# Kernel optimization log

Measured on AMD Instinct MI355X. Metric: run time of the kernel, lower is better.

The kernel has to match this reference:

```python
import jax, jax.numpy as jnp
import numpy as np

N_NODES = 100_000
N_EDGES = 1_600_000
N_FEAT = 128
N_HID = 64
N_CLASS = 10
N_LAYERS = 3
N_GRAPHS = 1000


def _linear_init(key, fan_in, fan_out):
    kw, kb = jax.random.split(key)
    s = 1.0 / np.sqrt(fan_in)
    w = jax.random.uniform(kw, (fan_in, fan_out), minval=-s, maxval=s, dtype=jnp.float32)
    b = jax.random.uniform(kb, (fan_out,), minval=-s, maxval=s, dtype=jnp.float32)
    return w, b


def setup_inputs() -> dict:
    key = jax.random.key(0)
    ks = jax.random.split(key, 16)
    x = jax.random.normal(ks[0], (N_NODES, N_FEAT), dtype=jnp.float32)
    edge_index = jax.random.randint(ks[1], (2, N_EDGES), 0, N_NODES, dtype=jnp.int64)
    batch = jnp.sort(jax.random.randint(ks[2], (N_NODES,), 0, N_GRAPHS, dtype=jnp.int64))

    pre_w, pre_b = _linear_init(ks[3], N_FEAT, N_HID)
    w1s, b1s, w2s, b2s = [], [], [], []
    for l in range(N_LAYERS):
        w1, b1 = _linear_init(jax.random.fold_in(ks[4], 2 * l), N_HID, N_HID)
        w2, b2 = _linear_init(jax.random.fold_in(ks[4], 2 * l + 1), N_HID, N_HID)
        w1s.append(w1); b1s.append(b1); w2s.append(w2); b2s.append(b2)
    post_w, post_b = _linear_init(ks[5], N_HID, N_HID)
    ro_w, ro_b = _linear_init(ks[6], N_HID, N_CLASS)

    return {
        "x": x, "edge_index": edge_index, "batch": batch,
        "pre_w": pre_w, "pre_b": pre_b,
        "conv_w1": jnp.stack(w1s), "conv_b1": jnp.stack(b1s),
        "conv_w2": jnp.stack(w2s), "conv_b2": jnp.stack(b2s),
        "post_w": post_w, "post_b": post_b,
        "ro_w": ro_w, "ro_b": ro_b,
    }


def reference(x, edge_index, batch, pre_w, pre_b, conv_w1, conv_b1, conv_w2, conv_b2, post_w, post_b, ro_w, ro_b):
    src = edge_index[0]  # message source (x_j)
    dst = edge_index[1]  # message target

    h = x @ pre_w + pre_b  # [N, H]
    for l in range(N_LAYERS):
        # GINConv, eps=0: MLP((1+eps)*h_i + sum_{j in N(i)} h_j)
        agg = jax.ops.segment_sum(h[src], dst, num_segments=N_NODES)
        z = h + agg
        z = jax.nn.relu(z @ conv_w1[l] + conv_b1[l]) @ conv_w2[l] + conv_b2[l]
        h = jax.nn.relu(z)  # dropout is identity in eval mode

    g = jax.ops.segment_sum(h, batch, num_segments=N_GRAPHS)  # global_add_pool [G, H]
    g = jax.nn.relu(g @ post_w + post_b)
    logits = g @ ro_w + ro_b
    return jax.nn.log_softmax(logits, axis=1)
```

## Files before the change

### kernel.cpp

```cpp
#include <hip/hip_runtime.h>
#include <math.h>

#define N_NODES  100000
#define N_FEAT   128
#define N_HID    64
#define N_CLASS  10
#define N_GRAPHS 1000
#define N_EDGES  1600000
#define NTILES   1563
#define BLK_N    128
#define NT2      782
#define HF_GROUPS 8
#define HF_RANGE 12500
#define HF_BLOCKS 2048
#define CSR_STRIDE 64
#define EMAX_LDS 32
#define APITCH 72

typedef int iv4 __attribute__((ext_vector_type(4)));
typedef __attribute__((ext_vector_type(8))) __bf16 bf16x8;
typedef __attribute__((ext_vector_type(4))) float f32x4;

__device__ __forceinline__ float bflo(unsigned u) { return __uint_as_float(u << 16); }
__device__ __forceinline__ float bfhi(unsigned u) { return __uint_as_float(u & 0xffff0000u); }
__device__ __forceinline__ unsigned bf_rne(float f) {
    unsigned u = __float_as_uint(f);
    return (u + 0x7fffu + ((u >> 16) & 1u)) >> 16;
}
__device__ __forceinline__ unsigned pack2(float a, float b) {
    return bf_rne(a) | (bf_rne(b) << 16);
}

__global__ __launch_bounds__(256, 4) void pre_kernel(
    const float* __restrict__ x, const float* __restrict__ W,
    const float* __restrict__ b, uint2* __restrict__ h)
{
    __shared__ float xs[64][68];
    __shared__ float ws[64][68];
    const int tid = threadIdx.x;
    const int tx = tid & 15, ty = tid >> 4;
    const int n0 = blockIdx.x * 64;

    float acc[4][4];
#pragma unroll
    for (int i = 0; i < 4; ++i)
#pragma unroll
        for (int j = 0; j < 4; ++j) acc[i][j] = 0.f;

    for (int p = 0; p < 2; ++p) {
        __syncthreads();
#pragma unroll
        for (int t = 0; t < 4; ++t) {
            const int idx = t * 256 + tid;
            const int m = idx >> 4, kv = idx & 15;
            float4 v = make_float4(0.f, 0.f, 0.f, 0.f);
            if (n0 + m < N_NODES)
                v = *(const float4*)(x + (size_t)(n0 + m) * N_FEAT + p * 64 + kv * 4);
            *(float4*)&xs[m][kv * 4] = v;
            *(float4*)&ws[m][kv * 4] =
                *(const float4*)(W + (size_t)(p * 64 + m) * N_HID + kv * 4);
        }
        __syncthreads();
#pragma unroll 2
        for (int k4 = 0; k4 < 16; ++k4) {
            float4 a[4], bb[4];
#pragma unroll
            for (int i = 0; i < 4; ++i)
                a[i] = *(const float4*)&xs[ty + 16 * i][k4 * 4];
#pragma unroll
            for (int j = 0; j < 4; ++j)
                bb[j] = *(const float4*)&ws[k4 * 4 + j][tx * 4];
#pragma unroll
            for (int i = 0; i < 4; ++i) {
                const float* ap = (const float*)&a[i];
#pragma unroll
                for (int j = 0; j < 4; ++j) {
                    const float* bp = (const float*)&bb[j];
#pragma unroll
                    for (int c = 0; c < 4; ++c)
                        acc[i][c] = fmaf(ap[j], bp[c], acc[i][c]);
                }
            }
        }
    }

    const float4 bias = *(const float4*)(b + tx * 4);
#pragma unroll
    for (int i = 0; i < 4; ++i) {
        const int node = n0 + ty + 16 * i;
        if (node < N_NODES) {
            h[(size_t)node * 16 + tx] = make_uint2(
                pack2(acc[i][0] + bias.x, acc[i][1] + bias.y),
                pack2(acc[i][2] + bias.z, acc[i][3] + bias.w));
        }
    }
}

__global__ __launch_bounds__(256) void hist_fill_kernel(
    const int* __restrict__ ei, int* __restrict__ deg, int* __restrict__ csr)
{
    const int r   = blockIdx.x & (HF_GROUPS - 1);
    const int g   = blockIdx.x >> 3;
    const int lo  = r * HF_RANGE;
    const int hi  = lo + HF_RANGE;
    const int gsz = (gridDim.x >> 3) * blockDim.x;
    const int t0  = g * blockDim.x + threadIdx.x;
    const iv4* dst4 = (const iv4*)(ei + N_EDGES);
    for (int q = t0; q < N_EDGES / 4; q += gsz) {
        const iv4 d = __builtin_nontemporal_load(dst4 + q);
        const int e0 = q * 4;
        if (d.x >= lo && d.x < hi) {
            int p = atomicAdd(&deg[d.x], 1);
            if (p < CSR_STRIDE)
                csr[d.x * CSR_STRIDE + p] = __builtin_nontemporal_load(ei + e0);
        }
        if (d.y >= lo && d.y < hi) {
            int p = atomicAdd(&deg[d.y], 1);
            if (p < CSR_STRIDE)
                csr[d.y * CSR_STRIDE + p] = __builtin_nontemporal_load(ei + e0 + 1);
        }
        if (d.z >= lo && d.z < hi) {
            int p = atomicAdd(&deg[d.z], 1);
            if (p < CSR_STRIDE)
                csr[d.z * CSR_STRIDE + p] = __builtin_nontemporal_load(ei + e0 + 2);
        }
        if (d.w >= lo && d.w < hi) {
            int p = atomicAdd(&deg[d.w], 1);
            if (p < CSR_STRIDE)
                csr[d.w * CSR_STRIDE + p] = __builtin_nontemporal_load(ei + e0 + 3);
        }
    }
}

__global__ __launch_bounds__(512, 6) void gather_mlp_kernel(
    const uint2* __restrict__ hin, uint2* __restrict__ hout,
    const int* __restrict__ csr, const int* __restrict__ deg,
    const float* __restrict__ W1, const float* __restrict__ b1,
    const float* __restrict__ W2, const float* __restrict__ b2)
{
    __shared__ unsigned short asb[BLK_N][APITCH];
    __shared__ unsigned short wsb[N_HID][APITCH];
    __shared__ int sdeg[BLK_N];
    const int tid = threadIdx.x;
    const int tx = tid & 15, ty = tid >> 4;
    const int sub = tx;
    const int n0 = blockIdx.x * BLK_N;

#pragma unroll
    for (int t = 0; t < 8; ++t) {
        const int idx = t * 512 + tid;
        wsb[idx & 63][idx >> 6] = (unsigned short)bf_rne(W1[idx]);
    }
    if (tid < BLK_N) {
        const int node = n0 + tid;
        sdeg[tid] = (node < N_NODES) ? deg[node] : 0;
    }
#pragma unroll
    for (int t = 0; t < 2; ++t) {
        const int idx = t * 512 + tid;
        const int r = idx >> 3, s4 = idx & 7;
        const int node = n0 + r;
        int4 v = make_int4(0, 0, 0, 0);
        if (node < N_NODES)
            v = *(const int4*)(csr + (size_t)node * CSR_STRIDE + s4 * 4);
        *(int4*)((char*)&asb[r][0] + s4 * 16) = v;
    }
    __syncthreads();

    for (int pp = 0; pp < 2; ++pp) {
        const int rA = ty + 64 * pp;
        const int rB = rA + 32;
        const int nodeA = n0 + rA;
        const int nodeB = n0 + rB;
        float aAx = 0.f, aAy = 0.f, aAz = 0.f, aAw = 0.f;
        float bAx = 0.f, bAy = 0.f, bAz = 0.f, bAw = 0.f;
        float aBx = 0.f, aBy = 0.f, aBz = 0.f, aBw = 0.f;
        float bBx = 0.f, bBy = 0.f, bBz = 0.f, bBw = 0.f;
        int nA = 0, nB = 0;
        if (nodeA < N_NODES) {
            nA = sdeg[rA]; nA = nA > CSR_STRIDE ? CSR_STRIDE : nA;
            const uint2 s = hin[(size_t)nodeA * 16 + sub];
            aAx = bflo(s.x); aAy = bfhi(s.x); aAz = bflo(s.y); aAw = bfhi(s.y);
        }
        if (nodeB < N_NODES) {
            nB = sdeg[rB]; nB = nB > CSR_STRIDE ? CSR_STRIDE : nB;
            const uint2 s = hin[(size_t)nodeB * 16 + sub];
            aBx = bflo(s.x); aBy = bfhi(s.x); aBz = bflo(s.y); aBw = bfhi(s.y);
        }
        const int nnA = nA > EMAX_LDS ? EMAX_LDS : nA;
        const int nnB = nB > EMAX_LDS ? EMAX_LDS : nB;
        const int* epA = (const int*)&asb[rA][0];
        const int* epB = (const int*)&asb[rB][0];
        const int mx = nnA > nnB ? nnA : nnB;
        for (int eb = 0; eb < mx; eb += 8) {
            uint2 rvA[8], rvB[8];
            const bool doA = eb < nnA;
            const bool doB = eb < nnB;
            if (doA) {
#pragma unroll
                for (int u = 0; u < 8; ++u) {
                    const int idx = eb + u;
                    const int cl = idx < nnA ? idx : nnA - 1;
                    rvA[u] = hin[(size_t)epA[cl] * 16 + sub];
                }
            }
            if (doB) {
#pragma unroll
                for (int u = 0; u < 8; ++u) {
                    const int idx = eb + u;
                    const int cl = idx < nnB ? idx : nnB - 1;
                    rvB[u] = hin[(size_t)epB[cl] * 16 + sub];
                }
            }
            if (doA) {
#pragma unroll
                for (int u = 0; u < 8; u += 2) {
                    if (eb + u < nnA) {
                        aAx += bflo(rvA[u].x); aAy += bfhi(rvA[u].x);
                        aAz += bflo(rvA[u].y); aAw += bfhi(rvA[u].y);
                    }
                    if (eb + u + 1 < nnA) {
                        bAx += bflo(rvA[u + 1].x); bAy += bfhi(rvA[u + 1].x);
                        bAz += bflo(rvA[u + 1].y); bAw += bfhi(rvA[u + 1].y);
                    }
                }
            }
            if (doB) {
#pragma unroll
                for (int u = 0; u < 8; u += 2) {
                    if (eb + u < nnB) {
                        aBx += bflo(rvB[u].x); aBy += bfhi(rvB[u].x);
                        aBz += bflo(rvB[u].y); aBw += bfhi(rvB[u].y);
                    }
                    if (eb + u + 1 < nnB) {
                        bBx += bflo(rvB[u + 1].x); bBy += bfhi(rvB[u + 1].x);
                        bBz += bflo(rvB[u + 1].y); bBw += bfhi(rvB[u + 1].y);
                    }
                }
            }
        }
        for (int t = EMAX_LDS; t < nA; ++t) {
            const int s0 = csr[(size_t)nodeA * CSR_STRIDE + t];
            const uint2 a = hin[(size_t)s0 * 16 + sub];
            aAx += bflo(a.x); aAy += bfhi(a.x);
            aAz += bflo(a.y); aAw += bfhi(a.y);
        }
        for (int t = EMAX_LDS; t < nB; ++t) {
            const int s0 = csr[(size_t)nodeB * CSR_STRIDE + t];
            const uint2 a = hin[(size_t)s0 * 16 + sub];
            aBx += bflo(a.x); aBy += bfhi(a.x);
            aBz += bflo(a.y); aBw += bfhi(a.y);
        }
        *(uint2*)((char*)&asb[rA][0] + sub * 8) = make_uint2(
            pack2(aAx + bAx, aAy + bAy), pack2(aAz + bAz, aAw + bAw));
        *(uint2*)((char*)&asb[rB][0] + sub * 8) = make_uint2(
            pack2(aBx + bBx, aBy + bBy), pack2(aBz + bBz, aBw + bBw));
    }
    __syncthreads();

    const int wave = tid >> 6;
    const int lane = tid & 63;
    const int lr = lane & 15;
    const int lg = lane >> 4;
    const f32x4 vzero = {0.f, 0.f, 0.f, 0.f};

    f32x4 acc[4] = {vzero, vzero, vzero, vzero};
    {
        const char* ar = (const char*)&asb[wave * 16 + lr][0] + lg * 16;
        const bf16x8 a0 = *(const bf16x8*)ar;
        const bf16x8 a1 = *(const bf16x8*)(ar + 64);
#pragma unroll
        for (int cb = 0; cb < 4; ++cb) {
            const char* br = (const char*)&wsb[cb * 16 + lr][0] + lg * 16;
            const bf16x8 w0 = *(const bf16x8*)br;
            const bf16x8 w1 = *(const bf16x8*)(br + 64);
            acc[cb] = __builtin_amdgcn_mfma_f32_16x16x32_bf16(a0, w0, acc[cb], 0, 0, 0);
            acc[cb] = __builtin_amdgcn_mfma_f32_16x16x32_bf16(a1, w1, acc[cb], 0, 0, 0);
        }
    }
#pragma unroll
    for (int cb = 0; cb < 4; ++cb) {
        const float bias = b1[cb * 16 + lr];
#pragma unroll
        for (int rg = 0; rg < 4; ++rg) {
            const float v = fmaxf(acc[cb][rg] + bias, 0.f);
            asb[wave * 16 + lg * 4 + rg][cb * 16 + lr] = (unsigned short)bf_rne(v);
        }
    }
    __syncthreads();
#pragma unroll
    for (int t = 0; t < 8; ++t) {
        const int idx = t * 512 + tid;
        wsb[idx & 63][idx >> 6] = (unsigned short)bf_rne(W2[idx]);
    }
    __syncthreads();

#pragma unroll
    for (int cb = 0; cb < 4; ++cb) acc[cb] = vzero;
    {
        const char* ar = (const char*)&asb[wave * 16 + lr][0] + lg * 16;
        const bf16x8 a0 = *(const bf16x8*)ar;
        const bf16x8 a1 = *(const bf16x8*)(ar + 64);
#pragma unroll
        for (int cb = 0; cb < 4; ++cb) {
            const char* br = (const char*)&wsb[cb * 16 + lr][0] + lg * 16;
            const bf16x8 w0 = *(const bf16x8*)br;
            const bf16x8 w1 = *(const bf16x8*)(br + 64);
            acc[cb] = __builtin_amdgcn_mfma_f32_16x16x32_bf16(a0, w0, acc[cb], 0, 0, 0);
            acc[cb] = __builtin_amdgcn_mfma_f32_16x16x32_bf16(a1, w1, acc[cb], 0, 0, 0);
        }
    }
#pragma unroll
    for (int cb = 0; cb < 4; ++cb) {
        const float bias = b2[cb * 16 + lr];
#pragma unroll
        for (int rg = 0; rg < 4; ++rg) {
            const float v = fmaxf(acc[cb][rg] + bias, 0.f);
            asb[wave * 16 + lg * 4 + rg][cb * 16 + lr] = (unsigned short)bf_rne(v);
        }
    }
    __syncthreads();

#pragma unroll
    for (int t = 0; t < 4; ++t) {
        const int idx = t * 512 + tid;
        const int m = idx >> 4, kv = idx & 15;
        if (n0 + m < N_NODES)
            hout[(size_t)(n0 + m) * 16 + kv] =
                *(const uint2*)((const char*)&asb[m][0] + kv * 8);
    }
}

__global__ __launch_bounds__(256) void pool_head_kernel(
    const unsigned short* __restrict__ h, const int* __restrict__ batch,
    const float* __restrict__ Wp, const float* __restrict__ bp,
    const float* __restrict__ Wr, const float* __restrict__ br,
    float* __restrict__ out)
{
    const int graph = blockIdx.x;
    int l = 0, r = N_NODES;
    while (l < r) { int m = (l + r) >> 1; if (batch[m] < graph) l = m + 1; else r = m; }
    const int lo = l;
    r = N_NODES;
    while (l < r) { int m = (l + r) >> 1; if (batch[m] < graph + 1) l = m + 1; else r = m; }
    const int hi = l;

    const int lane = threadIdx.x & 63;
    const int wave = threadIdx.x >> 6;
    float acc = 0.0f;
    for (int i = lo + wave; i < hi; i += 4)
        acc += __uint_as_float(((unsigned)h[(size_t)i * N_HID + lane]) << 16);
    __shared__ float sacc[4][N_HID];
    sacc[wave][lane] = acc;
    __syncthreads();
    if (wave != 0) return;

    const float gv = sacc[0][lane] + sacc[1][lane] + sacc[2][lane] + sacc[3][lane];
    float acc2 = bp[lane];
#pragma unroll
    for (int k = 0; k < N_HID; ++k) {
        const float gk = __int_as_float(
            __builtin_amdgcn_readlane(__float_as_int(gv), k));
        acc2 = fmaf(gk, Wp[k * N_HID + lane], acc2);
    }
    const float y = fmaxf(acc2, 0.f);

    float logit = (lane < N_CLASS) ? br[lane] : 0.f;
#pragma unroll
    for (int k = 0; k < N_HID; ++k) {
        const float yk = __int_as_float(
            __builtin_amdgcn_readlane(__float_as_int(y), k));
        if (lane < N_CLASS)
            logit = fmaf(yk, Wr[k * N_CLASS + lane], logit);
    }

    __shared__ float slog[N_CLASS];
    if (lane < N_CLASS) slog[lane] = logit;
    if (lane < N_CLASS) {
        float m = -INFINITY;
#pragma unroll
        for (int c = 0; c < N_CLASS; ++c) m = fmaxf(m, slog[c]);
        float sum = 0.0f;
#pragma unroll
        for (int c = 0; c < N_CLASS; ++c) sum += expf(slog[c] - m);
        out[(size_t)graph * N_CLASS + lane] = logit - m - logf(sum);
    }
}

extern "C" void kernel_launch(void* const* d_in, const int* in_sizes, int n_in,
                              void* d_out, int out_size, void* d_ws, size_t ws_size,
                              hipStream_t stream)
{
    const float* x       = (const float*)d_in[0];
    const int*   ei      = (const int*)d_in[1];
    const int*   batch   = (const int*)d_in[2];
    const float* pre_w   = (const float*)d_in[3];
    const float* pre_b   = (const float*)d_in[4];
    const float* conv_w1 = (const float*)d_in[5];
    const float* conv_b1 = (const float*)d_in[6];
    const float* conv_w2 = (const float*)d_in[7];
    const float* conv_b2 = (const float*)d_in[8];
    const float* post_w  = (const float*)d_in[9];
    const float* post_b  = (const float*)d_in[10];
    const float* ro_w    = (const float*)d_in[11];
    const float* ro_b    = (const float*)d_in[12];
    float* out = (float*)d_out;

    uint2* h0   = (uint2*)d_ws;
    uint2* h1   = h0 + (size_t)N_NODES * 16;
    int*   deg  = (int*)(h1 + (size_t)N_NODES * 16);
    int*   csr  = deg + N_NODES;

    (void)hipMemsetAsync(deg, 0, N_NODES * sizeof(int), stream);

    pre_kernel<<<NTILES, 256, 0, stream>>>(x, pre_w, pre_b, h0);
    hist_fill_kernel<<<HF_BLOCKS, 256, 0, stream>>>(ei, deg, csr);

    gather_mlp_kernel<<<NT2, 512, 0, stream>>>(
        h0, h1, csr, deg,
        conv_w1, conv_b1, conv_w2, conv_b2);
    gather_mlp_kernel<<<NT2, 512, 0, stream>>>(
        h1, h0, csr, deg,
        conv_w1 + N_HID * N_HID, conv_b1 + N_HID,
        conv_w2 + N_HID * N_HID, conv_b2 + N_HID);
    gather_mlp_kernel<<<NT2, 512, 0, stream>>>(
        h0, h1, csr, deg,
        conv_w1 + 2 * N_HID * N_HID, conv_b1 + 2 * N_HID,
        conv_w2 + 2 * N_HID * N_HID, conv_b2 + 2 * N_HID);

    pool_head_kernel<<<N_GRAPHS, 256, 0, stream>>>(
        (const unsigned short*)h1, batch, post_w, post_b, ro_w, ro_b, out);
}
```

Measured before the change: 379.1 us.

## Fuse pre-linear and CSR histogram fill into one interleaved kernel

Merges the pre-projection GEMM and the edge histogram/CSR fill into a single launch, interleaving the two block types so the compute-bound projection and the atomic-heavy CSR build share the GPU at the same time. The pre-projection is rewritten so each wavefront holds 16 node rows in registers and broadcasts x values with readlane, with no LDS tiling. This drops a launch and its tail, and lets the two independent phases overlap. The cost is higher register pressure and a less efficient per-wave FMA scheme: there are 16 readlanes per k, and W is reloaded from global memory per k.

```diff
diff --git a/kernel.cpp b/kernel.cpp
--- a/kernel.cpp
+++ b/kernel.cpp
@@ -13,6 +13,8 @@
 #define HF_GROUPS 8
 #define HF_RANGE 12500
 #define HF_BLOCKS 2048
+#define HF_GSZ   65536
+#define FUSED_BLOCKS (2*NTILES + (HF_BLOCKS - NTILES))
 #define CSR_STRIDE 64
 #define EMAX_LDS 32
 #define APITCH 72
@@ -31,103 +33,84 @@
     return bf_rne(a) | (bf_rne(b) << 16);
 }
 
-__global__ __launch_bounds__(256, 4) void pre_kernel(
+__global__ __launch_bounds__(256, 6) void pre_hist_kernel(
     const float* __restrict__ x, const float* __restrict__ W,
-    const float* __restrict__ b, uint2* __restrict__ h)
-{
-    __shared__ float xs[64][68];
-    __shared__ float ws[64][68];
-    const int tid = threadIdx.x;
-    const int tx = tid & 15, ty = tid >> 4;
-    const int n0 = blockIdx.x * 64;
-
-    float acc[4][4];
-#pragma unroll
-    for (int i = 0; i < 4; ++i)
-#pragma unroll
-        for (int j = 0; j < 4; ++j) acc[i][j] = 0.f;
-
-    for (int p = 0; p < 2; ++p) {
-        __syncthreads();
-#pragma unroll
-        for (int t = 0; t < 4; ++t) {
-            const int idx = t * 256 + tid;
-            const int m = idx >> 4, kv = idx & 15;
-            float4 v = make_float4(0.f, 0.f, 0.f, 0.f);
-            if (n0 + m < N_NODES)
-                v = *(const float4*)(x + (size_t)(n0 + m) * N_FEAT + p * 64 + kv * 4);
-            *(float4*)&xs[m][kv * 4] = v;
-            *(float4*)&ws[m][kv * 4] =
-                *(const float4*)(W + (size_t)(p * 64 + m) * N_HID + kv * 4);
-        }
-        __syncthreads();
-#pragma unroll 2
-        for (int k4 = 0; k4 < 16; ++k4) {
-            float4 a[4], bb[4];
-#pragma unroll
-            for (int i = 0; i < 4; ++i)
-                a[i] = *(const float4*)&xs[ty + 16 * i][k4 * 4];
-#pragma unroll
-            for (int j = 0; j < 4; ++j)
-                bb[j] = *(const float4*)&ws[k4 * 4 + j][tx * 4];
-#pragma unroll
-            for (int i = 0; i < 4; ++i) {
-                const float* ap = (const float*)&a[i];
-#pragma unroll
-                for (int j = 0; j < 4; ++j) {
-                    const float* bp = (const float*)&bb[j];
-#pragma unroll
-                    for (int c = 0; c < 4; ++c)
-                        acc[i][c] = fmaf(ap[j], bp[c], acc[i][c]);
-                }
-            }
-        }
-    }
-
-    const float4 bias = *(const float4*)(b + tx * 4);
-#pragma unroll
-    for (int i = 0; i < 4; ++i) {
-        const int node = n0 + ty + 16 * i;
-        if (node < N_NODES) {
-            h[(size_t)node * 16 + tx] = make_uint2(
-                pack2(acc[i][0] + bias.x, acc[i][1] + bias.y),
-                pack2(acc[i][2] + bias.z, acc[i][3] + bias.w));
-        }
-    }
-}
-
-__global__ __launch_bounds__(256) void hist_fill_kernel(
+    const float* __restrict__ b, unsigned short* __restrict__ h16,
     const int* __restrict__ ei, int* __restrict__ deg, int* __restrict__ csr)
 {
-    const int r   = blockIdx.x & (HF_GROUPS - 1);
-    const int g   = blockIdx.x >> 3;
-    const int lo  = r * HF_RANGE;
-    const int hi  = lo + HF_RANGE;
-    const int gsz = (gridDim.x >> 3) * blockDim.x;
-    const int t0  = g * blockDim.x + threadIdx.x;
-    const iv4* dst4 = (const iv4*)(ei + N_EDGES);
-    for (int q = t0; q < N_EDGES / 4; q += gsz) {
-        const iv4 d = __builtin_nontemporal_load(dst4 + q);
-        const int e0 = q * 4;
-        if (d.x >= lo && d.x < hi) {
-            int p = atomicAdd(&deg[d.x], 1);
-            if (p < CSR_STRIDE)
-                csr[d.x * CSR_STRIDE + p] = __builtin_nontemporal_load(ei + e0);
-        }
-        if (d.y >= lo && d.y < hi) {
-            int p = atomicAdd(&deg[d.y], 1);
-            if (p < CSR_STRIDE)
-                csr[d.y * CSR_STRIDE + p] = __builtin_nontemporal_load(ei + e0 + 1);
-        }
-        if (d.z >= lo && d.z < hi) {
-            int p = atomicAdd(&deg[d.z], 1);
-            if (p < CSR_STRIDE)
-                csr[d.z * CSR_STRIDE + p] = __builtin_nontemporal_load(ei + e0 + 2);
-        }
-        if (d.w >= lo && d.w < hi) {
-            int p = atomicAdd(&deg[d.w], 1);
-            if (p < CSR_STRIDE)
-                csr[d.w * CSR_STRIDE + p] = __builtin_nontemporal_load(ei + e0 + 3);
+    const int bi = blockIdx.x;
+    const int tid = threadIdx.x;
+    int prei = -1, hb = -1;
+    if (bi < 2 * NTILES) {
+        if ((bi & 1) == 0) prei = bi >> 1;
+        else hb = bi >> 1;
+    } else {
+        hb = NTILES + (bi - 2 * NTILES);
+    }
+
+    if (prei >= 0) {
+        const int lane = tid & 63;
+        const int wv = tid >> 6;
+        const int nb = prei * 64 + wv * 16;
+        float xr[32];
+        float acc[16];
+#pragma unroll
+        for (int i = 0; i < 16; ++i) acc[i] = 0.f;
+#pragma unroll
+        for (int i = 0; i < 16; ++i) {
+            const int node = nb + i;
+            const bool ok = node < N_NODES;
+            xr[2 * i]     = ok ? x[(size_t)node * N_FEAT + lane]      : 0.f;
+            xr[2 * i + 1] = ok ? x[(size_t)node * N_FEAT + 64 + lane] : 0.f;
+        }
+#pragma unroll
+        for (int k = 0; k < 128; ++k) {
+            const float wk = W[k * N_HID + lane];
+#pragma unroll
+            for (int i = 0; i < 16; ++i) {
+                const float xk = __int_as_float(__builtin_amdgcn_readlane(
+                    __float_as_int(xr[2 * i + (k >> 6)]), k & 63));
+                acc[i] = fmaf(xk, wk, acc[i]);
+            }
+        }
+        const float bias = b[lane];
+#pragma unroll
+        for (int i = 0; i < 16; ++i) {
+            const int node = nb + i;
+            if (node < N_NODES)
+                h16[(size_t)node * N_HID + lane] =
+                    (unsigned short)bf_rne(acc[i] + bias);
+        }
+    } else {
+        const int r   = hb & (HF_GROUPS - 1);
+        const int g   = hb >> 3;
+        const int lo  = r * HF_RANGE;
+        const int hi  = lo + HF_RANGE;
+        const int t0  = g * 256 + tid;
+        const iv4* dst4 = (const iv4*)(ei + N_EDGES);
+        for (int q = t0; q < N_EDGES / 4; q += HF_GSZ) {
+            const iv4 d = __builtin_nontemporal_load(dst4 + q);
+            const int e0 = q * 4;
+            if (d.x >= lo && d.x < hi) {
+                int p = atomicAdd(&deg[d.x], 1);
+                if (p < CSR_STRIDE)
+                    csr[d.x * CSR_STRIDE + p] = __builtin_nontemporal_load(ei + e0);
+            }
+            if (d.y >= lo && d.y < hi) {
+                int p = atomicAdd(&deg[d.y], 1);
+                if (p < CSR_STRIDE)
+                    csr[d.y * CSR_STRIDE + p] = __builtin_nontemporal_load(ei + e0 + 1);
+            }
+            if (d.z >= lo && d.z < hi) {
+                int p = atomicAdd(&deg[d.z], 1);
+                if (p < CSR_STRIDE)
+                    csr[d.z * CSR_STRIDE + p] = __builtin_nontemporal_load(ei + e0 + 2);
+            }
+            if (d.w >= lo && d.w < hi) {
+                int p = atomicAdd(&deg[d.w], 1);
+                if (p < CSR_STRIDE)
+                    csr[d.w * CSR_STRIDE + p] = __builtin_nontemporal_load(ei + e0 + 3);
+            }
         }
     }
 }
@@ -413,8 +396,8 @@
 
     (void)hipMemsetAsync(deg, 0, N_NODES * sizeof(int), stream);
 
-    pre_kernel<<<NTILES, 256, 0, stream>>>(x, pre_w, pre_b, h0);
-    hist_fill_kernel<<<HF_BLOCKS, 256, 0, stream>>>(ei, deg, csr);
+    pre_hist_kernel<<<FUSED_BLOCKS, 256, 0, stream>>>(
+        x, pre_w, pre_b, (unsigned short*)h0, ei, deg, csr);
 
     gather_mlp_kernel<<<NT2, 512, 0, stream>>>(
         h0, h1, csr, deg,
```

Measured after the change: 1.204 ms. 218% more time.
